# Kernel optimization log

Measured on AMD Instinct MI355X. Metric: run time of the kernel, lower is better.

The kernel has to match this reference:

```python
import jax, jax.numpy as jnp
import numpy as np

MAGIC = np.int32(1597463007)  # 0x5f3759df, Quake fast inverse sqrt constant

def fast_inv_sqrt(v):
    # v: [..., 1] float32. Bit-trick initial guess + one Newton iteration.
    x2 = v * 0.5
    i = jax.lax.bitcast_convert_type(v, jnp.int32)
    i = MAGIC - (i >> 1)
    y = jax.lax.bitcast_convert_type(i, jnp.float32)
    # Original detaches y (the bit-trick guess); only x2 carries gradient.
    y = jax.lax.stop_gradient(y)
    return y * (1.5 - x2 * y * y)

def setup_inputs() -> dict:
    key = jax.random.key(0)
    k1, = jax.random.split(key, 1)
    B, S, H = 8, 8192, 1024
    x = jax.random.normal(k1, (B, S, H), dtype=jnp.float32)
    weight = jnp.ones((H,), dtype=jnp.float32)
    bias = jnp.zeros((H,), dtype=jnp.float32)
    return {"x": x, "weight": weight, "bias": bias}

def reference(x, weight, bias):
    eps = 1e-05
    mean = jnp.mean(x, axis=-1, keepdims=True)
    var = jnp.var(x, axis=-1, keepdims=True)  # unbiased=False
    sr_inv = fast_inv_sqrt(var + eps)
    xn = (x - mean) * sr_inv
    return weight * xn + bias
```

## Files before the change

### kernel.cpp

```cpp
#include <hip/hip_runtime.h>


#define H 1024
#define THREADS 256

__device__ __forceinline__ float fast_inv_sqrt_dev(float v) {
    float x2 = v * 0.5f;
    int i = __float_as_int(v);
    i = 1597463007 - (i >> 1);
    float y = __int_as_float(i);
    return y * (1.5f - x2 * y * y);
}

__global__ __launch_bounds__(THREADS) void srnorm_kernel(
    const float* __restrict__ x,
    const float* __restrict__ weight,
    const float* __restrict__ bias,
    float* __restrict__ out)
{
    const int row = blockIdx.x;
    const int tid = threadIdx.x;
    const size_t base = (size_t)row * H;

    const float4 v = reinterpret_cast<const float4*>(x + base)[tid];

    float s  = v.x + v.y + v.z + v.w;
    float sq = v.x * v.x + v.y * v.y + v.z * v.z + v.w * v.w;

    #pragma unroll
    for (int off = 32; off > 0; off >>= 1) {
        s  += __shfl_down(s,  off, 64);
        sq += __shfl_down(sq, off, 64);
    }

    __shared__ float ssum[4];
    __shared__ float ssq[4];
    const int wave = tid >> 6;
    const int lane = tid & 63;
    if (lane == 0) { ssum[wave] = s; ssq[wave] = sq; }
    __syncthreads();

    const float tot   = ssum[0] + ssum[1] + ssum[2] + ssum[3];
    const float totsq = ssq[0]  + ssq[1]  + ssq[2]  + ssq[3];

    const float mean = tot * (1.0f / (float)H);
    const float var  = totsq * (1.0f / (float)H) - mean * mean;
    const float sr   = fast_inv_sqrt_dev(var + 1e-5f);

    const float4 wv = reinterpret_cast<const float4*>(weight)[tid];
    const float4 bv = reinterpret_cast<const float4*>(bias)[tid];

    float4 o;
    o.x = wv.x * ((v.x - mean) * sr) + bv.x;
    o.y = wv.y * ((v.y - mean) * sr) + bv.y;
    o.z = wv.z * ((v.z - mean) * sr) + bv.z;
    o.w = wv.w * ((v.w - mean) * sr) + bv.w;

    reinterpret_cast<float4*>(out + base)[tid] = o;
}

extern "C" void kernel_launch(void* const* d_in, const int* in_sizes, int n_in,
                              void* d_out, int out_size, void* d_ws, size_t ws_size,
                              hipStream_t stream) {
    const float* x      = (const float*)d_in[0];
    const float* weight = (const float*)d_in[1];
    const float* bias   = (const float*)d_in[2];
    float* out = (float*)d_out;

    const int rows = in_sizes[0] / H;
    srnorm_kernel<<<rows, THREADS, 0, stream>>>(x, weight, bias, out);
}
```

Before: 98.83 us.

## Use persistent wave-per-row grid with nontemporal loads and stores

Each 64-lane wave now processes a whole row, with 16 floats per lane, in a grid-stride loop over a fixed grid of 2048 blocks. The row reduction becomes a pure xor-shuffle, which removes the LDS exchange and the block barrier. Weight and bias are loaded once per wave and kept in registers instead of being reloaded per row. Loads and stores use nontemporal hints to reduce cache pollution on this streaming pattern. The trade-offs are higher register use per lane and less memory-level parallelism per wave for each row.

```diff
diff --git a/kernel.cpp b/kernel.cpp
--- a/kernel.cpp
+++ b/kernel.cpp
@@ -3,6 +3,9 @@
 
 #define H 1024
 #define THREADS 256
+#define BLOCKS 2048
+
+typedef float f32x4 __attribute__((ext_vector_type(4)));
 
 __device__ __forceinline__ float fast_inv_sqrt_dev(float v) {
     float x2 = v * 0.5f;
@@ -16,47 +19,50 @@
     const float* __restrict__ x,
     const float* __restrict__ weight,
     const float* __restrict__ bias,
-    float* __restrict__ out)
+    float* __restrict__ out,
+    int rows)
 {
-    const int row = blockIdx.x;
-    const int tid = threadIdx.x;
-    const size_t base = (size_t)row * H;
+    const int lane   = threadIdx.x & 63;
+    const int wave   = blockIdx.x * (THREADS / 64) + (threadIdx.x >> 6);
+    const int nwaves = gridDim.x * (THREADS / 64);
 
-    const float4 v = reinterpret_cast<const float4*>(x + base)[tid];
-
-    float s  = v.x + v.y + v.z + v.w;
-    float sq = v.x * v.x + v.y * v.y + v.z * v.z + v.w * v.w;
-
+    f32x4 wv[4], bv[4];
     #pragma unroll
-    for (int off = 32; off > 0; off >>= 1) {
-        s  += __shfl_down(s,  off, 64);
-        sq += __shfl_down(sq, off, 64);
+    for (int k = 0; k < 4; ++k) {
+        wv[k] = reinterpret_cast<const f32x4*>(weight)[lane + k * 64];
+        bv[k] = reinterpret_cast<const f32x4*>(bias)[lane + k * 64];
     }
 
-    __shared__ float ssum[4];
-    __shared__ float ssq[4];
-    const int wave = tid >> 6;
-    const int lane = tid & 63;
-    if (lane == 0) { ssum[wave] = s; ssq[wave] = sq; }
-    __syncthreads();
+    for (int row = wave; row < rows; row += nwaves) {
+        const f32x4* xr = reinterpret_cast<const f32x4*>(x + (size_t)row * H);
+        f32x4*       orow = reinterpret_cast<f32x4*>(out + (size_t)row * H);
 
-    const float tot   = ssum[0] + ssum[1] + ssum[2] + ssum[3];
-    const float totsq = ssq[0]  + ssq[1]  + ssq[2]  + ssq[3];
+        f32x4 v[4];
+        float s = 0.0f, sq = 0.0f;
+        #pragma unroll
+        for (int k = 0; k < 4; ++k) {
+            v[k] = __builtin_nontemporal_load(xr + lane + k * 64);
+            s  += v[k].x + v[k].y + v[k].z + v[k].w;
+            sq += v[k].x * v[k].x + v[k].y * v[k].y
+                + v[k].z * v[k].z + v[k].w * v[k].w;
+        }
 
-    const float mean = tot * (1.0f / (float)H);
-    const float var  = totsq * (1.0f / (float)H) - mean * mean;
-    const float sr   = fast_inv_sqrt_dev(var + 1e-5f);
+        #pragma unroll
+        for (int off = 32; off > 0; off >>= 1) {
+            s  += __shfl_xor(s,  off, 64);
+            sq += __shfl_xor(sq, off, 64);
+        }
 
-    const float4 wv = reinterpret_cast<const float4*>(weight)[tid];
-    const float4 bv = reinterpret_cast<const float4*>(bias)[tid];
+        const float mean = s * (1.0f / (float)H);
+        const float var  = sq * (1.0f / (float)H) - mean * mean;
+        const float sr   = fast_inv_sqrt_dev(var + 1e-5f);
 
-    float4 o;
-    o.x = wv.x * ((v.x - mean) * sr) + bv.x;
-    o.y = wv.y * ((v.y - mean) * sr) + bv.y;
-    o.z = wv.z * ((v.z - mean) * sr) + bv.z;
-    o.w = wv.w * ((v.w - mean) * sr) + bv.w;
-
-    reinterpret_cast<float4*>(out + base)[tid] = o;
+        #pragma unroll
+        for (int k = 0; k < 4; ++k) {
+            f32x4 o = wv[k] * ((v[k] - mean) * sr) + bv[k];
+            __builtin_nontemporal_store(o, orow + lane + k * 64);
+        }
+    }
 }
 
 extern "C" void kernel_launch(void* const* d_in, const int* in_sizes, int n_in,
@@ -68,5 +74,5 @@
     float* out = (float*)d_out;
 
     const int rows = in_sizes[0] / H;
-    srnorm_kernel<<<rows, THREADS, 0, stream>>>(x, weight, bias, out);
+    srnorm_kernel<<<BLOCKS, THREADS, 0, stream>>>(x, weight, bias, out, rows);
 }
```

Result: faster. 94.41 us (-4.5%).
